# Optimization experiments

Measured on AMD Instinct MI355X. Metric: run time of the kernel, lower is better.

## Reference

```python
import jax, jax.numpy as jnp
import numpy as np

BINS = 64
MIN_VAL, MAX_VAL = 0.0, 1.0


def soft_histogram(x, bins=BINS, min_val=MIN_VAL, max_val=MAX_VAL):
    # x: (B, C, H, W)
    B, C, H, W = x.shape
    x_flat = x.reshape(B, C, -1)                       # (B, C, HW)
    bin_width = (max_val - min_val) / bins
    centers = jnp.linspace(min_val + bin_width / 2, max_val - bin_width / 2, bins,
                           dtype=x.dtype)              # (bins,)
    sigma = bin_width
    # broadcasted Gaussian kernel weights, reduced over pixels -> (B, C, bins)
    diff = x_flat[..., None] - centers                 # (B, C, HW, bins)
    weights = jnp.exp(-(diff ** 2) / (2.0 * sigma ** 2))
    hist = weights.sum(axis=2)                         # (B, C, bins)
    hist = hist / (hist.sum(axis=-1, keepdims=True) + 1e-8)
    return hist


def setup_inputs() -> dict:
    key = jax.random.key(0)
    k1, k2 = jax.random.split(key)
    pred = jax.random.uniform(k1, (4, 3, 256, 256), dtype=jnp.float32)
    target = jax.random.uniform(k2, (4, 3, 256, 256), dtype=jnp.float32)
    return {"pred": pred, "target": target}


def reference(pred, target):
    pred_hist = soft_histogram(pred, BINS)
    target_hist = soft_histogram(target, BINS)
    pred_cdf = jnp.cumsum(pred_hist, axis=-1)
    target_cdf = jnp.cumsum(target_hist, axis=-1)
    return jnp.mean(jnp.abs(pred_cdf - target_cdf))
```

## Files before the change

### kernel.cpp

```cpp
#include <hip/hip_runtime.h>


#define BINS 64
#define NCH 12
#define HW 65536
#define BPC 32
#define PIX_PER_BLOCK (HW / BPC)
#define THREADS 128
#define PPT (PIX_PER_BLOCK / THREADS)
#define R 6
#define WIN (2 * R + 1)
#define PADBINS (BINS + 2 * R)
#define NW (THREADS / 64)

__device__ __forceinline__ float fast_exp2(float x) {
#if __has_builtin(__builtin_amdgcn_exp2f)
    return __builtin_amdgcn_exp2f(x);
#else
    return exp2f(x);
#endif
}

__global__ __launch_bounds__(THREADS) void hist_kernel(
        const float* __restrict__ pred,
        const float* __restrict__ target,
        float* __restrict__ part_out) {
    constexpr float CK[WIN] = {
        1.5229979744712628e-08f, 3.7266531720786709e-06f,
        3.3546262790251185e-04f, 1.1108996538242306e-02f,
        1.3533528323661270e-01f, 6.0653065971263342e-01f, 1.0f,
        6.0653065971263342e-01f, 1.3533528323661270e-01f,
        1.1108996538242306e-02f, 3.3546262790251185e-04f,
        3.7266531720786709e-06f, 1.5229979744712628e-08f };

    const int blk   = blockIdx.x;
    const int ch    = blk / BPC;
    const int chunk = blk % BPC;
    const float* src = (ch < NCH) ? (pred + (size_t)ch * HW)
                                  : (target + (size_t)(ch - NCH) * HW);

    __shared__ float h[NW][PADBINS][64];
    __shared__ float part[NW][BINS];

    const int wv   = threadIdx.x >> 6;
    const int lane = threadIdx.x & 63;

    {
        float4* hz = (float4*)&h[0][0][0];
        #pragma unroll
        for (int t = 0; t < NW * PADBINS * 64 / 4 / THREADS; ++t)
            hz[threadIdx.x + t * THREADS] = make_float4(0.f, 0.f, 0.f, 0.f);
    }
    __syncthreads();

    const float4* src4 = (const float4*)(src + chunk * PIX_PER_BLOCK);
    float4 a = src4[threadIdx.x];
    float4 b = src4[threadIdx.x + THREADS];
    float4 c = src4[threadIdx.x + 2 * THREADS];
    float4 d = src4[threadIdx.x + 3 * THREADS];
    float px[PPT] = {a.x, a.y, a.z, a.w, b.x, b.y, b.z, b.w,
                     c.x, c.y, c.z, c.w, d.x, d.y, d.z, d.w};

    const float L = 1.4426950408889634f;

    #pragma unroll
    for (int p = 0; p < PPT; ++p) {
        float xt = px[p] * 64.0f - 0.5f;
        float fi = rintf(xt);
        fi = fminf(fmaxf(fi, 0.0f), 63.0f);
        float f  = xt - fi;
        int   i  = (int)fi;
        float P  = fast_exp2(-(0.5f * L) * (f * f + (float)(2 * R) * f));
        float B  = fast_exp2(L * f);
        #pragma unroll
        for (int t = 0; t < WIN; ++t) {
            h[wv][i + t][lane] += CK[t] * P;
            P *= B;
        }
    }

    __syncthreads();

    {
        const int j = lane;
        float s = 0.0f;
        #pragma unroll
        for (int cc = 0; cc < 64; ++cc)
            s += h[wv][R + j][(j + cc) & 63];
        part[wv][j] = s;
    }
    __syncthreads();
    if (threadIdx.x < BINS) {
        const int j = threadIdx.x;
        part_out[blk * BINS + j] = part[0][j] + part[1][j];
    }
}

__global__ __launch_bounds__(NCH * 64) void final_kernel(
        const float* __restrict__ part, float* __restrict__ out) {
    const int w    = threadIdx.x >> 6;
    const int lane = threadIdx.x & 63;

    float ph = 0.0f, th = 0.0f;
    #pragma unroll
    for (int c = 0; c < BPC; ++c) {
        ph += part[(w * BPC + c) * BINS + lane];
        th += part[((NCH + w) * BPC + c) * BINS + lane];
    }

    float ps = ph, ts = th;
    #pragma unroll
    for (int d = 1; d < 64; d <<= 1) {
        float a = __shfl_up(ps, d, 64);
        float b = __shfl_up(ts, d, 64);
        if (lane >= d) { ps += a; ts += b; }
    }
    float ptot = __shfl(ps, 63, 64);
    float ttot = __shfl(ts, 63, 64);
    float pc = ps / (ptot + 1e-8f);
    float tc = ts / (ttot + 1e-8f);
    float dv = fabsf(pc - tc);

    #pragma unroll
    for (int k = 32; k >= 1; k >>= 1) dv += __shfl_xor(dv, k, 64);

    __shared__ float warr[NCH];
    if (lane == 0) warr[w] = dv;
    __syncthreads();
    if (threadIdx.x == 0) {
        float s = 0.0f;
        #pragma unroll
        for (int i = 0; i < NCH; ++i) s += warr[i];
        out[0] = s / (float)(NCH * BINS);
    }
}

extern "C" void kernel_launch(void* const* d_in, const int* in_sizes, int n_in,
                              void* d_out, int out_size, void* d_ws, size_t ws_size,
                              hipStream_t stream) {
    const float* pred   = (const float*)d_in[0];
    const float* target = (const float*)d_in[1];
    float* part = (float*)d_ws;
    float* out  = (float*)d_out;

    hist_kernel<<<dim3(2 * NCH * BPC), dim3(THREADS), 0, stream>>>(
        pred, target, part);
    final_kernel<<<dim3(1), dim3(NCH * 64), 0, stream>>>(part, out);
}
```

Baseline: 65.42 us.

## Transpose per-lane histogram layout and use paired float2 LDS updates

Switches the shared-memory histogram from bin-major with lanes as columns to lane-major rows padded to 84 floats. Each pixel now updates 12 bins through six float2 read-modify-writes aligned to an even window start, instead of 13 scalar updates. The aim is to halve the number of LDS instructions per pixel and to simplify the exponent setup. The padded row stride changes the bank-conflict pattern for both the scatter and the final transposed reduction, and the window now drops one tail weight whose side depends on the even alignment.

```diff
diff --git a/kernel.cpp b/kernel.cpp
--- a/kernel.cpp
+++ b/kernel.cpp
@@ -8,10 +8,9 @@
 #define PIX_PER_BLOCK (HW / BPC)
 #define THREADS 128
 #define PPT (PIX_PER_BLOCK / THREADS)
-#define R 6
-#define WIN (2 * R + 1)
-#define PADBINS (BINS + 2 * R)
+#define ROWPAD 84
 #define NW (THREADS / 64)
+#define WROWS 12
 
 __device__ __forceinline__ float fast_exp2(float x) {
 #if __has_builtin(__builtin_amdgcn_exp2f)
@@ -25,13 +24,14 @@
         const float* __restrict__ pred,
         const float* __restrict__ target,
         float* __restrict__ part_out) {
-    constexpr float CK[WIN] = {
-        1.5229979744712628e-08f, 3.7266531720786709e-06f,
-        3.3546262790251185e-04f, 1.1108996538242306e-02f,
-        1.3533528323661270e-01f, 6.0653065971263342e-01f, 1.0f,
+    constexpr float CC[WROWS] = {
+        1.0f,
         6.0653065971263342e-01f, 1.3533528323661270e-01f,
         1.1108996538242306e-02f, 3.3546262790251185e-04f,
-        3.7266531720786709e-06f, 1.5229979744712628e-08f };
+        3.7266531720786709e-06f, 1.5229979744712628e-08f,
+        2.2897348456455526e-11f, 1.2664165549094176e-14f,
+        2.5767571091549810e-18f, 1.9287498479639178e-22f,
+        5.3204056952276910e-27f };
 
     const int blk   = blockIdx.x;
     const int ch    = blk / BPC;
@@ -39,7 +39,7 @@
     const float* src = (ch < NCH) ? (pred + (size_t)ch * HW)
                                   : (target + (size_t)(ch - NCH) * HW);
 
-    __shared__ float h[NW][PADBINS][64];
+    __shared__ float h[NW][64][ROWPAD];
     __shared__ float part[NW][BINS];
 
     const int wv   = threadIdx.x >> 6;
@@ -48,7 +48,7 @@
     {
         float4* hz = (float4*)&h[0][0][0];
         #pragma unroll
-        for (int t = 0; t < NW * PADBINS * 64 / 4 / THREADS; ++t)
+        for (int t = 0; t < NW * 64 * ROWPAD / 4 / THREADS; ++t)
             hz[threadIdx.x + t * THREADS] = make_float4(0.f, 0.f, 0.f, 0.f);
     }
     __syncthreads();
@@ -61,21 +61,29 @@
     float px[PPT] = {a.x, a.y, a.z, a.w, b.x, b.y, b.z, b.w,
                      c.x, c.y, c.z, c.w, d.x, d.y, d.z, d.w};
 
-    const float L = 1.4426950408889634f;
+    const float L  = 1.4426950408889634f;
+    const float L2 = 0.7213475204444817f;
+
+    float2* lane2 = reinterpret_cast<float2*>(&h[wv][lane][0]);
 
     #pragma unroll
     for (int p = 0; p < PPT; ++p) {
         float xt = px[p] * 64.0f - 0.5f;
         float fi = rintf(xt);
         fi = fminf(fmaxf(fi, 0.0f), 63.0f);
-        float f  = xt - fi;
         int   i  = (int)fi;
-        float P  = fast_exp2(-(0.5f * L) * (f * f + (float)(2 * R) * f));
-        float B  = fast_exp2(L * f);
+        int   w0 = (i - 5) & ~1;
+        float f0 = xt - (float)w0;
+        float A  = fast_exp2(-L2 * f0 * f0);
+        float B  = fast_exp2(L * f0);
+        float P  = A;
+        int   b2 = (w0 + 6) >> 1;
         #pragma unroll
-        for (int t = 0; t < WIN; ++t) {
-            h[wv][i + t][lane] += CK[t] * P;
-            P *= B;
+        for (int s2 = 0; s2 < WROWS / 2; ++s2) {
+            float2 v = lane2[b2 + s2];
+            v.x = fmaf(P, CC[2 * s2], v.x);     P *= B;
+            v.y = fmaf(P, CC[2 * s2 + 1], v.y); P *= B;
+            lane2[b2 + s2] = v;
         }
     }
 
@@ -86,7 +94,7 @@
         float s = 0.0f;
         #pragma unroll
         for (int cc = 0; cc < 64; ++cc)
-            s += h[wv][R + j][(j + cc) & 63];
+            s += h[wv][(j + cc) & 63][j + 6];
         part[wv][j] = s;
     }
     __syncthreads();
```

Result: slower. 70.77 us (+8.2%).
